# Kernel optimization log

Hardware: AMD Instinct MI355X
Metric: run time of the kernel (lower is better)

The kernel has to match this reference:

```python
import jax, jax.numpy as jnp
import numpy as np

ALPHA = 16.0

def setup_inputs() -> dict:
    key = jax.random.key(0)
    k1, k2, k3, k4, k5 = jax.random.split(key, 5)
    B_, S, D_in, D_out, R = 4, 4096, 4096, 4096, 16
    x = jax.random.normal(k1, (B_, S, D_in), dtype=jnp.float32)
    W = jax.random.normal(k2, (D_out, D_in), dtype=jnp.float32) * 0.02
    A = jax.random.normal(k3, (R, D_in), dtype=jnp.float32) * 0.02
    Bm = jax.random.normal(k4, (D_out, R), dtype=jnp.float32) * 0.02
    bias = jax.random.normal(k5, (D_out,), dtype=jnp.float32)
    return {"x": x, "W": W, "A": A, "B": Bm, "bias": bias}

def reference(x, W, A, B, bias):
    # weight = W + (B @ A) * alpha ; out = x @ weight.T + bias
    weight = W + (B @ A) * ALPHA          # [D_out, D_in]
    return jnp.einsum('bsi,oi->bso', x, weight) + bias
```

## Files before the change

### kernel.cpp

```cpp
#include <hip/hip_runtime.h>
#include <hip/hip_bf16.h>

typedef short bf16x8 __attribute__((ext_vector_type(8)));
typedef short s16x4 __attribute__((ext_vector_type(4)));
typedef float f32x4 __attribute__((ext_vector_type(4)));

static constexpr int MTOT = 16384;
static constexpr int NDIM = 4096;
static constexpr int KDIM = 4096;
static constexpr int NKT  = KDIM / 64;
static constexpr float LORA_ALPHA = 16.0f;

static constexpr size_t OFF_AXH = 0;
static constexpr size_t OFF_AXL = OFF_AXH + (size_t)MTOT * KDIM * 2;
static constexpr size_t OFF_WH  = OFF_AXL + (size_t)MTOT * KDIM * 2;
static constexpr size_t OFF_WL  = OFF_WH  + (size_t)NDIM * KDIM * 2;
static constexpr size_t OFF_T   = OFF_WL  + (size_t)NDIM * KDIM * 2;
static constexpr size_t WS_NEED = OFF_T + (size_t)MTOT * 16 * 4;

__device__ __forceinline__ unsigned bf16rn_bits(float v) {
  unsigned b = __float_as_uint(v);
  return (b + 0x7FFFu + ((b >> 16) & 1u)) >> 16;
}

__device__ __forceinline__ void split4(const float4 v, s16x4& h, s16x4& l) {
  float f[4] = {v.x, v.y, v.z, v.w};
  #pragma unroll
  for (int e = 0; e < 4; ++e) {
    unsigned hb = bf16rn_bits(f[e]);
    float hf = __uint_as_float(hb << 16);
    float lv = f[e] - hf;
    h[e] = (short)hb;
    l[e] = (short)bf16rn_bits(lv);
  }
}

typedef __attribute__((address_space(3))) unsigned int lds_u32;
typedef __attribute__((address_space(1))) const unsigned int glb_u32;
__device__ __forceinline__ void gl2lds16(const short* g, short* l) {
  __builtin_amdgcn_global_load_lds((glb_u32*)g, (lds_u32*)l, 16, 0, 0);
}

__global__ __launch_bounds__(256) void convert_split_kernel(
    const float* __restrict__ src, short* __restrict__ dh,
    short* __restrict__ dl) {
  const size_t e = (size_t)blockIdx.x * 256 + threadIdx.x;
  const int m  = (int)(e >> 9);
  const int c8 = (int)(e & 511);
  const int k  = c8 << 3;
  const float* p = src + ((size_t)m << 12) + k;
  float4 v0 = *(const float4*)p;
  float4 v1 = *(const float4*)(p + 4);
  s16x4 h0, l0, h1, l1;
  split4(v0, h0, l0);
  split4(v1, h1, l1);
  const int rtile = m >> 7, row = m & 127, ktile = k >> 6, kin = k & 63;
  const size_t base = ((size_t)rtile * NKT + ktile) * 8192;
  const int idx = row * 64 + (kin ^ ((row & 7) << 3));
  bf16x8 h = {h0[0], h0[1], h0[2], h0[3], h1[0], h1[1], h1[2], h1[3]};
  bf16x8 l = {l0[0], l0[1], l0[2], l0[3], l1[0], l1[1], l1[2], l1[3]};
  *(bf16x8*)&dh[base + idx] = h;
  *(bf16x8*)&dl[base + idx] = l;
}

__global__ __launch_bounds__(256) void lora_T_kernel(
    const float* __restrict__ x, const float* __restrict__ A,
    float* __restrict__ T) {
  const int wave = threadIdx.x >> 6;
  const int lane = threadIdx.x & 63;
  const int m0 = blockIdx.x * 16 + wave * 4;

  float acc[4][16];
  #pragma unroll
  for (int i = 0; i < 4; ++i)
    #pragma unroll
    for (int r = 0; r < 16; ++r) acc[i][r] = 0.f;

  for (int k0 = 0; k0 < KDIM; k0 += 256) {
    const int k = k0 + lane * 4;
    float4 xv[4];
    #pragma unroll
    for (int i = 0; i < 4; ++i)
      xv[i] = *(const float4*)&x[(size_t)(m0 + i) * KDIM + k];
    #pragma unroll
    for (int r = 0; r < 16; ++r) {
      float4 av = *(const float4*)&A[r * KDIM + k];
      #pragma unroll
      for (int i = 0; i < 4; ++i) {
        acc[i][r] += xv[i].x * av.x + xv[i].y * av.y +
                     xv[i].z * av.z + xv[i].w * av.w;
      }
    }
  }

  #pragma unroll
  for (int i = 0; i < 4; ++i)
    #pragma unroll
    for (int r = 0; r < 16; ++r) {
      float v = acc[i][r];
      #pragma unroll
      for (int off = 32; off; off >>= 1) v += __shfl_xor(v, off, 64);
      acc[i][r] = v;
    }

  const int i = lane >> 4, r = lane & 15;
  T[(size_t)(m0 + i) * 16 + r] = acc[i][r];
}

__global__ __launch_bounds__(512, 4) void lora_gemm_pre(
    const short* __restrict__ Axh, const short* __restrict__ Axl,
    const short* __restrict__ Wh,  const short* __restrict__ Wl,
    const float* __restrict__ Bm,  const float* __restrict__ bias,
    const float* __restrict__ T,   float* __restrict__ out) {

  __shared__ short smem[4 * 128 * 64];
  short* const sxh = smem;
  short* const sxl = smem + 8192;
  short* const swh = smem + 16384;
  short* const swl = smem + 24576;

  const int tid = threadIdx.x;
  const int per = gridDim.x >> 3;
  const int swz = (blockIdx.x & 7) * per + (blockIdx.x >> 3);
  const int bm = swz / (NDIM / 128);
  const int bn = swz % (NDIM / 128);

  const short* baseAh = Axh + ((size_t)bm * NKT) * 8192;
  const short* baseAl = Axl + ((size_t)bm * NKT) * 8192;
  const short* baseWh = Wh + ((size_t)bn * NKT) * 8192;
  const short* baseWl = Wl + ((size_t)bn * NKT) * 8192;

  const int lane = tid & 63;
  const int wave = tid >> 6;
  const int wm = wave >> 2, wn = wave & 3;
  const int frow = lane & 15;
  const int fk = (lane >> 4) * 8;

  f32x4 acc[4][2];
  #pragma unroll
  for (int i = 0; i < 4; ++i)
    #pragma unroll
    for (int j = 0; j < 2; ++j) acc[i][j] = (f32x4){0.f, 0.f, 0.f, 0.f};

  const int soff0 = tid * 8;
  const int soff1 = soff0 + 4096;

  for (int kt = 0; kt < NKT; ++kt) {
    __syncthreads();
    {
      const size_t tb = (size_t)kt * 8192;
      gl2lds16(baseAh + tb + soff0, sxh + soff0);
      gl2lds16(baseAh + tb + soff1, sxh + soff1);
      gl2lds16(baseAl + tb + soff0, sxl + soff0);
      gl2lds16(baseAl + tb + soff1, sxl + soff1);
      gl2lds16(baseWh + tb + soff0, swh + soff0);
      gl2lds16(baseWh + tb + soff1, swh + soff1);
      gl2lds16(baseWl + tb + soff0, swl + soff0);
      gl2lds16(baseWl + tb + soff1, swl + soff1);
    }
    __syncthreads();

    #pragma unroll
    for (int kk = 0; kk < 2; ++kk) {
      const int colk = kk * 32 + fk;
      bf16x8 ah[4], al[4], bh[2], bl[2];
      #pragma unroll
      for (int mt = 0; mt < 4; ++mt) {
        const int ra = wm * 64 + mt * 16 + frow;
        const int ia = ra * 64 + (colk ^ ((ra & 7) << 3));
        ah[mt] = *(const bf16x8*)&sxh[ia];
        al[mt] = *(const bf16x8*)&sxl[ia];
      }
      #pragma unroll
      for (int nt = 0; nt < 2; ++nt) {
        const int rb = wn * 32 + nt * 16 + frow;
        const int ib = rb * 64 + (colk ^ ((rb & 7) << 3));
        bh[nt] = *(const bf16x8*)&swh[ib];
        bl[nt] = *(const bf16x8*)&swl[ib];
      }
      #pragma unroll
      for (int mt = 0; mt < 4; ++mt)
        #pragma unroll
        for (int nt = 0; nt < 2; ++nt)
          acc[mt][nt] = __builtin_amdgcn_mfma_f32_16x16x32_bf16(ah[mt], bh[nt], acc[mt][nt], 0, 0, 0);
      #pragma unroll
      for (int mt = 0; mt < 4; ++mt)
        #pragma unroll
        for (int nt = 0; nt < 2; ++nt)
          acc[mt][nt] = __builtin_amdgcn_mfma_f32_16x16x32_bf16(al[mt], bh[nt], acc[mt][nt], 0, 0, 0);
      #pragma unroll
      for (int mt = 0; mt < 4; ++mt)
        #pragma unroll
        for (int nt = 0; nt < 2; ++nt)
          acc[mt][nt] = __builtin_amdgcn_mfma_f32_16x16x32_bf16(ah[mt], bl[nt], acc[mt][nt], 0, 0, 0);
    }
  }

  const int m0 = bm * 128 + wm * 64;
  const int n0 = bn * 128 + wn * 32;

  float4 brow[2][4];
  float bs[2];
  #pragma unroll
  for (int nt = 0; nt < 2; ++nt) {
    const int n = n0 + nt * 16 + frow;
    #pragma unroll
    for (int q = 0; q < 4; ++q)
      brow[nt][q] = *(const float4*)&Bm[n * 16 + q * 4];
    bs[nt] = bias[n];
  }

  const int rbase = (lane >> 4) * 4;
  #pragma unroll
  for (int mt = 0; mt < 4; ++mt) {
    #pragma unroll
    for (int r = 0; r < 4; ++r) {
      const int m = m0 + mt * 16 + rbase + r;
      float4 t4[4];
      #pragma unroll
      for (int q = 0; q < 4; ++q)
        t4[q] = *(const float4*)&T[(size_t)m * 16 + q * 4];
      #pragma unroll
      for (int nt = 0; nt < 2; ++nt) {
        float corr =
            t4[0].x * brow[nt][0].x + t4[0].y * brow[nt][0].y + t4[0].z * brow[nt][0].z + t4[0].w * brow[nt][0].w +
            t4[1].x * brow[nt][1].x + t4[1].y * brow[nt][1].y + t4[1].z * brow[nt][1].z + t4[1].w * brow[nt][1].w +
            t4[2].x * brow[nt][2].x + t4[2].y * brow[nt][2].y + t4[2].z * brow[nt][2].z + t4[2].w * brow[nt][2].w +
            t4[3].x * brow[nt][3].x + t4[3].y * brow[nt][3].y + t4[3].z * brow[nt][3].z + t4[3].w * brow[nt][3].w;
        out[(size_t)m * NDIM + n0 + nt * 16 + frow] =
            acc[mt][nt][r] + bs[nt] + LORA_ALPHA * corr;
      }
    }
  }
}

__global__ __launch_bounds__(256, 2) void lora_gemm_fallback(
    const float* __restrict__ x, const float* __restrict__ W,
    const float* __restrict__ Bm, const float* __restrict__ bias,
    const float* __restrict__ T, float* __restrict__ out) {

  __shared__ short smem[4 * 128 * 64];

  const int tid = threadIdx.x;
  const int per = gridDim.x >> 3;
  const int swz = (blockIdx.x & 7) * per + (blockIdx.x >> 3);
  const int bm = swz / (NDIM / 128);
  const int bn = swz % (NDIM / 128);

  const int srow = tid >> 4;
  const int sc4 = tid & 15;
  const float* xg = x + (size_t)(bm * 128 + srow) * KDIM + sc4 * 4;
  const float* wg = W + (size_t)(bn * 128 + srow) * KDIM + sc4 * 4;

  float4 xr[8], wr[8];

  auto loadTile = [&](int kt) {
    const float* xp = xg + kt * 64;
    const float* wp = wg + kt * 64;
    #pragma unroll
    for (int i = 0; i < 8; ++i) {
      xr[i] = *(const float4*)(xp + (size_t)(i * 16) * KDIM);
      wr[i] = *(const float4*)(wp + (size_t)(i * 16) * KDIM);
    }
  };

  auto writeTile = [&]() {
    #pragma unroll
    for (int i = 0; i < 8; ++i) {
      const int row = srow + i * 16;
      const int idx = row * 64 + ((sc4 * 4) ^ ((row & 7) << 3));
      s16x4 h, l;
      split4(xr[i], h, l);
      *(s16x4*)&smem[idx] = h;
      *(s16x4*)&smem[8192 + idx] = l;
      split4(wr[i], h, l);
      *(s16x4*)&smem[16384 + idx] = h;
      *(s16x4*)&smem[24576 + idx] = l;
    }
  };

  const int lane = tid & 63;
  const int wave = tid >> 6;
  const int wm = wave >> 1, wn = wave & 1;
  const int frow = lane & 15;
  const int fk = (lane >> 4) * 8;

  f32x4 acc[4][4];
  #pragma unroll
  for (int i = 0; i < 4; ++i)
    #pragma unroll
    for (int j = 0; j < 4; ++j) acc[i][j] = (f32x4){0.f, 0.f, 0.f, 0.f};

  loadTile(0);
  constexpr int NT = KDIM / 64;
  for (int kt = 0; kt < NT; ++kt) {
    __syncthreads();
    writeTile();
    __syncthreads();
    if (kt + 1 < NT) loadTile(kt + 1);

    #pragma unroll
    for (int kk = 0; kk < 2; ++kk) {
      const int colk = kk * 32 + fk;
      bf16x8 ah[4], al[4], bh[4], bl[4];
      #pragma unroll
      for (int t = 0; t < 4; ++t) {
        const int ra = wm * 64 + t * 16 + frow;
        const int ia = ra * 64 + (colk ^ ((ra & 7) << 3));
        ah[t] = *(const bf16x8*)&smem[ia];
        al[t] = *(const bf16x8*)&smem[8192 + ia];
        const int rb = wn * 64 + t * 16 + frow;
        const int ib = rb * 64 + (colk ^ ((rb & 7) << 3));
        bh[t] = *(const bf16x8*)&smem[16384 + ib];
        bl[t] = *(const bf16x8*)&smem[24576 + ib];
      }
      #pragma unroll
      for (int mt = 0; mt < 4; ++mt)
        #pragma unroll
        for (int nt = 0; nt < 4; ++nt) {
          acc[mt][nt] = __builtin_amdgcn_mfma_f32_16x16x32_bf16(ah[mt], bh[nt], acc[mt][nt], 0, 0, 0);
          acc[mt][nt] = __builtin_amdgcn_mfma_f32_16x16x32_bf16(al[mt], bh[nt], acc[mt][nt], 0, 0, 0);
          acc[mt][nt] = __builtin_amdgcn_mfma_f32_16x16x32_bf16(ah[mt], bl[nt], acc[mt][nt], 0, 0, 0);
        }
    }
  }

  const int m0 = bm * 128 + wm * 64;
  const int n0 = bn * 128 + wn * 64;

  float4 brow[4][4];
  float bs[4];
  #pragma unroll
  for (int nt = 0; nt < 4; ++nt) {
    const int n = n0 + nt * 16 + frow;
    #pragma unroll
    for (int q = 0; q < 4; ++q)
      brow[nt][q] = *(const float4*)&Bm[n * 16 + q * 4];
    bs[nt] = bias[n];
  }

  const int rbase = (lane >> 4) * 4;
  #pragma unroll
  for (int mt = 0; mt < 4; ++mt) {
    #pragma unroll
    for (int r = 0; r < 4; ++r) {
      const int m = m0 + mt * 16 + rbase + r;
      float4 t4[4];
      #pragma unroll
      for (int q = 0; q < 4; ++q)
        t4[q] = *(const float4*)&T[(size_t)m * 16 + q * 4];
      #pragma unroll
      for (int nt = 0; nt < 4; ++nt) {
        float corr =
            t4[0].x * brow[nt][0].x + t4[0].y * brow[nt][0].y + t4[0].z * brow[nt][0].z + t4[0].w * brow[nt][0].w +
            t4[1].x * brow[nt][1].x + t4[1].y * brow[nt][1].y + t4[1].z * brow[nt][1].z + t4[1].w * brow[nt][1].w +
            t4[2].x * brow[nt][2].x + t4[2].y * brow[nt][2].y + t4[2].z * brow[nt][2].z + t4[2].w * brow[nt][2].w +
            t4[3].x * brow[nt][3].x + t4[3].y * brow[nt][3].y + t4[3].z * brow[nt][3].z + t4[3].w * brow[nt][3].w;
        out[(size_t)m * NDIM + n0 + nt * 16 + frow] =
            acc[mt][nt][r] + bs[nt] + LORA_ALPHA * corr;
      }
    }
  }
}

extern "C" void kernel_launch(void* const* d_in, const int* in_sizes, int n_in,
                              void* d_out, int out_size, void* d_ws, size_t ws_size,
                              hipStream_t stream) {
  const float* x    = (const float*)d_in[0];
  const float* W    = (const float*)d_in[1];
  const float* A    = (const float*)d_in[2];
  const float* Bm   = (const float*)d_in[3];
  const float* bias = (const float*)d_in[4];
  float* out = (float*)d_out;
  char* ws = (char*)d_ws;

  if (ws_size >= WS_NEED) {
    short* Axh = (short*)(ws + OFF_AXH);
    short* Axl = (short*)(ws + OFF_AXL);
    short* Wh  = (short*)(ws + OFF_WH);
    short* Wl  = (short*)(ws + OFF_WL);
    float* T   = (float*)(ws + OFF_T);

    hipLaunchKernelGGL(convert_split_kernel, dim3(NDIM * 2), dim3(256), 0,
                       stream, W, Wh, Wl);
    hipLaunchKernelGGL(convert_split_kernel, dim3(MTOT * 2), dim3(256), 0,
                       stream, x, Axh, Axl);
    hipLaunchKernelGGL(lora_T_kernel, dim3(MTOT / 16), dim3(256), 0, stream,
                       x, A, T);
    hipLaunchKernelGGL(lora_gemm_pre,
                       dim3((MTOT / 128) * (NDIM / 128)), dim3(512), 0, stream,
                       Axh, Axl, Wh, Wl, Bm, bias, T, out);
  } else {
    float* T = (float*)ws;
    hipLaunchKernelGGL(lora_T_kernel, dim3(MTOT / 16), dim3(256), 0, stream,
                       x, A, T);
    hipLaunchKernelGGL(lora_gemm_fallback,
                       dim3((MTOT / 128) * (NDIM / 128)), dim3(256), 0, stream,
                       x, W, Bm, bias, T, out);
  }
}
```

Measured before the change: 1.998 ms.

## Double-buffer LDS tiles in split-bf16 GEMM and remap conversion kernel stores

The main GEMM now keeps two LDS buffers and issues the global-to-LDS loads for the next K tile before computing on the current one. It waits with explicit vmcnt counts and raw barriers, so memory latency can overlap the MFMA work. Doubling LDS to 128KB per block drops the occupancy hint to one block per CU. The conversion kernel is also remapped so each wave writes a contiguous row segment of a swizzled tile across four K tiles, which should give more coalesced stores.

```diff
diff --git a/kernel.cpp b/kernel.cpp
--- a/kernel.cpp
+++ b/kernel.cpp
@@ -44,23 +44,29 @@
 __global__ __launch_bounds__(256) void convert_split_kernel(
     const float* __restrict__ src, short* __restrict__ dh,
     short* __restrict__ dl) {
-  const size_t e = (size_t)blockIdx.x * 256 + threadIdx.x;
-  const int m  = (int)(e >> 9);
-  const int c8 = (int)(e & 511);
-  const int k  = c8 << 3;
-  const float* p = src + ((size_t)m << 12) + k;
-  float4 v0 = *(const float4*)p;
-  float4 v1 = *(const float4*)(p + 4);
-  s16x4 h0, l0, h1, l1;
-  split4(v0, h0, l0);
-  split4(v1, h1, l1);
-  const int rtile = m >> 7, row = m & 127, ktile = k >> 6, kin = k & 63;
-  const size_t base = ((size_t)rtile * NKT + ktile) * 8192;
-  const int idx = row * 64 + (kin ^ ((row & 7) << 3));
-  bf16x8 h = {h0[0], h0[1], h0[2], h0[3], h1[0], h1[1], h1[2], h1[3]};
-  bf16x8 l = {l0[0], l0[1], l0[2], l0[3], l1[0], l1[1], l1[2], l1[3]};
-  *(bf16x8*)&dh[base + idx] = h;
-  *(bf16x8*)&dl[base + idx] = l;
+  const int wave = threadIdx.x >> 6;
+  const int lane = threadIdx.x & 63;
+  const int row = blockIdx.y * 32 + wave * 8 + (lane >> 3);
+  const int kin = (lane & 7) * 8;
+  const int rtile = row >> 7;
+  const int rloc = row & 127;
+  const int idx = rloc * 64 + (kin ^ ((rloc & 7) << 3));
+  const float* p = src + (size_t)row * KDIM + kin;
+  #pragma unroll
+  for (int t = 0; t < 4; ++t) {
+    const int kt = blockIdx.x * 4 + t;
+    const float* q = p + kt * 64;
+    float4 v0 = *(const float4*)q;
+    float4 v1 = *(const float4*)(q + 4);
+    s16x4 h0, l0, h1, l1;
+    split4(v0, h0, l0);
+    split4(v1, h1, l1);
+    const size_t base = ((size_t)rtile * NKT + kt) * 8192;
+    bf16x8 h = {h0[0], h0[1], h0[2], h0[3], h1[0], h1[1], h1[2], h1[3]};
+    bf16x8 l = {l0[0], l0[1], l0[2], l0[3], l1[0], l1[1], l1[2], l1[3]};
+    *(bf16x8*)&dh[base + idx] = h;
+    *(bf16x8*)&dl[base + idx] = l;
+  }
 }
 
 __global__ __launch_bounds__(256) void lora_T_kernel(
@@ -107,17 +113,13 @@
   T[(size_t)(m0 + i) * 16 + r] = acc[i][r];
 }
 
-__global__ __launch_bounds__(512, 4) void lora_gemm_pre(
+__global__ __launch_bounds__(512, 1) void lora_gemm_pre(
     const short* __restrict__ Axh, const short* __restrict__ Axl,
     const short* __restrict__ Wh,  const short* __restrict__ Wl,
     const float* __restrict__ Bm,  const float* __restrict__ bias,
     const float* __restrict__ T,   float* __restrict__ out) {
 
-  __shared__ short smem[4 * 128 * 64];
-  short* const sxh = smem;
-  short* const sxl = smem + 8192;
-  short* const swh = smem + 16384;
-  short* const swl = smem + 24576;
+  __shared__ short smem[2][4 * 8192];
 
   const int tid = threadIdx.x;
   const int per = gridDim.x >> 3;
@@ -145,20 +147,34 @@
   const int soff0 = tid * 8;
   const int soff1 = soff0 + 4096;
 
+  auto STAGE = [&](int kt, int buf) {
+    const size_t tb = (size_t)kt * 8192;
+    short* s = smem[buf];
+    gl2lds16(baseAh + tb + soff0, s + soff0);
+    gl2lds16(baseAh + tb + soff1, s + soff1);
+    gl2lds16(baseAl + tb + soff0, s + 8192 + soff0);
+    gl2lds16(baseAl + tb + soff1, s + 8192 + soff1);
+    gl2lds16(baseWh + tb + soff0, s + 16384 + soff0);
+    gl2lds16(baseWh + tb + soff1, s + 16384 + soff1);
+    gl2lds16(baseWl + tb + soff0, s + 24576 + soff0);
+    gl2lds16(baseWl + tb + soff1, s + 24576 + soff1);
+  };
+
+  STAGE(0, 0);
   for (int kt = 0; kt < NKT; ++kt) {
-    __syncthreads();
-    {
-      const size_t tb = (size_t)kt * 8192;
-      gl2lds16(baseAh + tb + soff0, sxh + soff0);
-      gl2lds16(baseAh + tb + soff1, sxh + soff1);
-      gl2lds16(baseAl + tb + soff0, sxl + soff0);
-      gl2lds16(baseAl + tb + soff1, sxl + soff1);
-      gl2lds16(baseWh + tb + soff0, swh + soff0);
-      gl2lds16(baseWh + tb + soff1, swh + soff1);
-      gl2lds16(baseWl + tb + soff0, swl + soff0);
-      gl2lds16(baseWl + tb + soff1, swl + soff1);
-    }
-    __syncthreads();
+    const int cur = kt & 1;
+    if (kt + 1 < NKT) {
+      STAGE(kt + 1, cur ^ 1);
+      asm volatile("s_waitcnt vmcnt(8)" ::: "memory");
+    } else {
+      asm volatile("s_waitcnt vmcnt(0)" ::: "memory");
+    }
+    __builtin_amdgcn_s_barrier();
+
+    const short* sxh = smem[cur];
+    const short* sxl = smem[cur] + 8192;
+    const short* swh = smem[cur] + 16384;
+    const short* swl = smem[cur] + 24576;
 
     #pragma unroll
     for (int kk = 0; kk < 2; ++kk) {
@@ -194,6 +210,9 @@
         for (int nt = 0; nt < 2; ++nt)
           acc[mt][nt] = __builtin_amdgcn_mfma_f32_16x16x32_bf16(ah[mt], bl[nt], acc[mt][nt], 0, 0, 0);
     }
+
+    asm volatile("" ::: "memory");
+    __builtin_amdgcn_s_barrier();
   }
 
   const int m0 = bm * 128 + wm * 64;
@@ -381,10 +400,10 @@
     short* Wl  = (short*)(ws + OFF_WL);
     float* T   = (float*)(ws + OFF_T);
 
-    hipLaunchKernelGGL(convert_split_kernel, dim3(NDIM * 2), dim3(256), 0,
-                       stream, W, Wh, Wl);
-    hipLaunchKernelGGL(convert_split_kernel, dim3(MTOT * 2), dim3(256), 0,
-                       stream, x, Axh, Axl);
+    hipLaunchKernelGGL(convert_split_kernel, dim3(NKT / 4, NDIM / 32),
+                       dim3(256), 0, stream, W, Wh, Wl);
+    hipLaunchKernelGGL(convert_split_kernel, dim3(NKT / 4, MTOT / 32),
+                       dim3(256), 0, stream, x, Axh, Axl);
     hipLaunchKernelGGL(lora_T_kernel, dim3(MTOT / 16), dim3(256), 0, stream,
                        x, A, T);
     hipLaunchKernelGGL(lora_gemm_pre,
```

New measurement: 2.358 ms. 1.18x slower.
